# Performance work log

Hardware: AMD Instinct MI355X
Metric: run time of the kernel (lower is better)

The kernel has to match this reference:

```python
import jax, jax.numpy as jnp
import numpy as np

B, T, IN = 128, 2048, 32      # batch, seq_len, input dim
S, M = 32, 8                  # kaarma state dim, number of ensemble models
E, H = 64, 128                # encoder dim, controller GRU hidden
CIN = E + 1                   # controller input = [encoded, error]


def setup_inputs() -> dict:
    key = jax.random.key(0)
    ks = jax.random.split(key, 15)
    sc = 0.1  # small init scale keeps tanh/sigmoid in sane range
    return {
        "x": jax.random.normal(ks[0], (B, T, IN), jnp.float32),
        "y": jax.random.normal(ks[1], (B, T), jnp.float32),
        # mkaarma params: shared encoder + per-model recurrent state update
        "W_enc": jax.random.normal(ks[2], (IN, E), jnp.float32) * sc,
        "b_enc": jnp.zeros((E,), jnp.float32),
        "W_in": jax.random.normal(ks[3], (M, IN, S), jnp.float32) * sc,
        "W_rec": jax.random.normal(ks[4], (M, S, S), jnp.float32) * sc,
        "b_s": jnp.zeros((M, S), jnp.float32),
        # controller params: GRU cell + gate head
        "W_x": jax.random.normal(ks[5], (CIN, 3 * H), jnp.float32) * sc,
        "W_h": jax.random.normal(ks[6], (H, 3 * H), jnp.float32) * sc,
        "b_x": jnp.zeros((3 * H,), jnp.float32),
        "b_h": jnp.zeros((3 * H,), jnp.float32),
        "W_gate": jax.random.normal(ks[7], (H, M), jnp.float32) * sc,
        "b_gate": jnp.zeros((M,), jnp.float32),
    }


def reference(x, y, W_enc, b_enc, W_in, W_rec, b_s,
              W_x, W_h, b_x, b_h, W_gate, b_gate):
    Bv = x.shape[0]
    dt = x.dtype

    def step(carry, xy):
        kstate, h, err = carry            # [B,S], [B,H], [B]
        x_t, y_t = xy                     # [B,IN], [B]
        # mkaarma: encode input + ensemble of candidate next states
        encoded = jnp.tanh(x_t @ W_enc + b_enc)                        # [B,E]
        new_state = jnp.tanh(
            jnp.einsum('bi,mis->bms', x_t, W_in)
            + jnp.einsum('bs,msd->bmd', kstate, W_rec)
            + b_s
        )                                                              # [B,M,S]
        # controller: GRU cell on [encoded, error]
        inp = jnp.concatenate([encoded, err[:, None]], axis=1)         # [B,E+1]
        xz, xr, xn = jnp.split(inp @ W_x + b_x, 3, axis=1)
        hz, hr, hn = jnp.split(h @ W_h + b_h, 3, axis=1)
        z = jax.nn.sigmoid(xz + hz)
        r = jax.nn.sigmoid(xr + hr)
        n = jnp.tanh(xn + r * hn)
        h_new = (1.0 - z) * n + z * h                                  # [B,H]
        # gate softmax over models, mix candidate states
        gate = jax.nn.softmax(h_new @ W_gate + b_gate, axis=1)         # [B,M]
        kstate_new = jnp.einsum('bm,bms->bs', gate, new_state)         # [B,S]
        pred = kstate_new[:, -1]                                       # [B]
        err_new = pred - y_t
        return (kstate_new, h_new, err_new), pred

    init = (jnp.zeros((Bv, S), dt), jnp.zeros((Bv, H), dt), jnp.zeros((Bv,), dt))
    xs = (jnp.swapaxes(x, 0, 1), jnp.swapaxes(y, 0, 1))   # time-major
    _, preds = jax.lax.scan(step, init, xs)               # [T,B]
    return jnp.swapaxes(preds, 0, 1)                      # [B,T]
```

## Files before the change

kernel.cpp:

```cpp
#include <hip/hip_runtime.h>

typedef _Float16 h2 __attribute__((ext_vector_type(2)));
typedef _Float16 h8 __attribute__((ext_vector_type(8)));

#define NB 128
#define NT 2048
#define NIN 32
#define NS 32
#define NM 8
#define NE 64
#define NH 128
#define NH3 384

__device__ __forceinline__ h2 mkh2(float a, float b) {
  h2 r; r[0] = (_Float16)a; r[1] = (_Float16)b; return r;
}

template <int I>
__device__ __forceinline__ h2 pick2(h8 v) {
  return __builtin_shufflevector(v, v, 2 * I, 2 * I + 1);
}

__device__ __forceinline__ float fdot2(h2 a, h2 b, float c) {
#if __has_builtin(__builtin_amdgcn_fdot2)
  return __builtin_amdgcn_fdot2(a, b, c, false);
#else
  return c + (float)a[0] * (float)b[0] + (float)a[1] * (float)b[1];
#endif
}

__device__ __forceinline__ float rcpf(float v) {
#if __has_builtin(__builtin_amdgcn_rcpf)
  return __builtin_amdgcn_rcpf(v);
#else
  return 1.0f / v;
#endif
}

__device__ __forceinline__ float sigmoid_f(float v) { return rcpf(1.0f + __expf(-v)); }
__device__ __forceinline__ float tanh_f(float v) { return 1.0f - 2.0f * rcpf(1.0f + __expf(2.0f * v)); }

template <int CTRL>
__device__ __forceinline__ float dppadd(float v) {
  int t = __builtin_amdgcn_update_dpp(0, __float_as_int(v), CTRL, 0xF, 0xF, true);
  return v + __int_as_float(t);
}
__device__ __forceinline__ float wave_reduce63(float v) {
  v = dppadd<0x111>(v); v = dppadd<0x112>(v); v = dppadd<0x114>(v);
  v = dppadd<0x118>(v); v = dppadd<0x142>(v); v = dppadd<0x143>(v);
  return v;
}
__device__ __forceinline__ float pairsum(float v) {
  int t = __builtin_amdgcn_update_dpp(0, __float_as_int(v), 0xB1, 0xF, 0xF, true);
  return v + __int_as_float(t);
}

__device__ __forceinline__ void lds_fence() {
  asm volatile("s_waitcnt lgkmcnt(0)" ::: "memory");
}

#define RPW 16
__global__ __launch_bounds__(256, 1) void pre2(
    const float* __restrict__ gx, const float* __restrict__ W_enc,
    const float* __restrict__ b_enc, const float* __restrict__ W_x,
    const float* __restrict__ b_x, _Float16* __restrict__ xpre,
    _Float16* __restrict__ xh16, int t0, int CH) {
  const int tid = threadIdx.x, wv = tid >> 6, lane = tid & 63;
  __shared__ __align__(16) _Float16 x16[4][NIN];
  __shared__ __align__(16) _Float16 encA[4][RPW][NE];

  h2 we[16];
#pragma unroll
  for (int i = 0; i < 16; ++i)
    we[i] = mkh2(W_enc[(2 * i) * NE + lane], W_enc[(2 * i + 1) * NE + lane]);
  const float be = b_enc[lane];

  const int g0 = ((int)blockIdx.x * 4 + wv) * RPW;

  h2 wx3[96];
#pragma unroll 1
  for (int pass = 0; pass < 2; ++pass) {
#pragma unroll
    for (int kk = 0; kk < 3; ++kk) {
      const int j = lane + 64 * (3 * pass + kk);
#pragma unroll
      for (int i = 0; i < 32; ++i)
        wx3[kk * 32 + i] = mkh2(W_x[(size_t)(2 * i) * NH3 + j], W_x[(size_t)(2 * i + 1) * NH3 + j]);
    }
#pragma unroll 1
    for (int r = 0; r < RPW; ++r) {
      const int g = g0 + r;
      const int bb = g / CH, tc = g % CH;
      if (pass == 0) {
        const float* xr = gx + ((size_t)bb * NT + t0 + tc) * NIN;
        if (lane < NIN) x16[wv][lane] = (_Float16)xr[lane];
        lds_fence();
        if (lane < 16) {
          const unsigned v = *(const unsigned*)&x16[wv][2 * lane];
          ((unsigned*)xh16)[(size_t)g * 16 + lane] = v;
        }
        const h8* xv8 = (const h8*)x16[wv];
        float a = be;
#pragma unroll
        for (int i = 0; i < 4; ++i) {
          const h8 xv = xv8[i];
          a = fdot2(pick2<0>(xv), we[4 * i + 0], a);
          a = fdot2(pick2<1>(xv), we[4 * i + 1], a);
          a = fdot2(pick2<2>(xv), we[4 * i + 2], a);
          a = fdot2(pick2<3>(xv), we[4 * i + 3], a);
        }
        encA[wv][r][lane] = (_Float16)tanh_f(a);
        lds_fence();
      }
      const h8* ev8 = (const h8*)encA[wv][r];
      h8 ev[8];
#pragma unroll
      for (int i = 0; i < 8; ++i) ev[i] = ev8[i];
#pragma unroll
      for (int kk = 0; kk < 3; ++kk) {
        const int j = lane + 64 * (3 * pass + kk);
        float a = b_x[j], c = 0.f;
#pragma unroll
        for (int i = 0; i < 8; ++i) {
          a = fdot2(pick2<0>(ev[i]), wx3[kk * 32 + 4 * i + 0], a);
          c = fdot2(pick2<1>(ev[i]), wx3[kk * 32 + 4 * i + 1], c);
          a = fdot2(pick2<2>(ev[i]), wx3[kk * 32 + 4 * i + 2], a);
          c = fdot2(pick2<3>(ev[i]), wx3[kk * 32 + 4 * i + 3], c);
        }
        xpre[(size_t)g * NH3 + j] = (_Float16)(a + c);
      }
    }
  }
}

__global__ __launch_bounds__(384, 2) void rnn3(
    const float* __restrict__ gy, const _Float16* __restrict__ xpre,
    const _Float16* __restrict__ xh16,
    const float* __restrict__ W_h, const float* __restrict__ b_h,
    const float* __restrict__ W_in, const float* __restrict__ W_rec,
    const float* __restrict__ b_s, const float* __restrict__ W_x,
    const float* __restrict__ W_gate, const float* __restrict__ b_gate,
    float* __restrict__ out, float* __restrict__ state, int t0, int CH) {
  const int tid = threadIdx.x;
  const int b = blockIdx.x;
  const int wv = tid >> 6;
  const int lane = tid & 63;

  __shared__ __align__(16) _Float16 h_sh[2][NH];
  __shared__ __align__(16) _Float16 xpre_sh[2][NH3];
  __shared__ __align__(16) float ns_sh[2][NS][NM];
  __shared__ __align__(16) float xd_sh[2][2 * NH];
  __shared__ __align__(16) float gp_sh[2][4][NM];
  __shared__ __align__(16) _Float16 kst_sh[NS];
  __shared__ float err_sh;

  float* st = state + b * (NH + NS + 1);

  h2 wbig[96];
  h2 wrec[16];
  float wg[8];
  float bh[3], wxe[3];
  float bs4[4];
  float bg[8];
  float h_prev = 0.f;
  float yp = 0.f, ym = 0.f;
  unsigned xpa0 = 0, xpa1 = 0, xpa2 = 0, xpb0 = 0, xpb1 = 0, xpb2 = 0;
  h8 xha[4], xhb[4];

  const int gl = tid - 128;
  const int j = gl >> 1;
  const int half = gl & 1;

  if (wv >= 2) {
#pragma unroll
    for (int g = 0; g < 3; ++g) {
      const int jc = j + 128 * g;
#pragma unroll
      for (int i = 0; i < 32; ++i)
        wbig[g * 32 + i] = mkh2(W_h[(size_t)(64 * half + 2 * i) * NH3 + jc],
                                W_h[(size_t)(64 * half + 2 * i + 1) * NH3 + jc]);
      bh[g] = b_h[jc];
      wxe[g] = W_x[(size_t)NE * NH3 + jc];
    }
#pragma unroll
    for (int m = 0; m < 8; ++m) wg[m] = half ? 0.f : W_gate[j * NM + m];
    {
      const int m0 = gl >> 5, d0 = gl & 31;
#pragma unroll
      for (int i = 0; i < 16; ++i)
        wrec[i] = mkh2(W_rec[m0 * 1024 + (2 * i) * 32 + d0],
                       W_rec[m0 * 1024 + (2 * i + 1) * 32 + d0]);
    }
    h_prev = t0 ? st[j] : 0.f;
    if (!half) h_sh[1][j] = (_Float16)h_prev;
  } else if (wv == 1) {
#pragma unroll
    for (int k = 0; k < 4; ++k) {
      const int o = lane + 64 * k, m = o >> 5, d = o & 31;
#pragma unroll
      for (int i = 0; i < 16; ++i)
        wbig[k * 16 + i] = mkh2(W_in[m * 1024 + (2 * i) * 32 + d],
                                W_in[m * 1024 + (2 * i + 1) * 32 + d]);
      bs4[k] = b_s[o];
    }
    const unsigned* xpg = (const unsigned*)xpre;
    {
      const size_t r0 = (size_t)(b * CH + 0) * 192;
      xpa0 = xpg[r0 + lane]; xpa1 = xpg[r0 + lane + 64]; xpa2 = xpg[r0 + lane + 128];
      const size_t r1 = (size_t)(b * CH + min(1, CH - 1)) * 192;
      xpb0 = xpg[r1 + lane]; xpb1 = xpg[r1 + lane + 64]; xpb2 = xpg[r1 + lane + 128];
    }
    {
      const h8* x0 = (const h8*)(xh16 + (size_t)(b * CH + 0) * NIN);
      h8 xv[4];
#pragma unroll
      for (int i = 0; i < 4; ++i) xv[i] = x0[i];
#pragma unroll
      for (int k = 0; k < 4; ++k) {
        float s = bs4[k];
#pragma unroll
        for (int i = 0; i < 4; ++i) {
          s = fdot2(pick2<0>(xv[i]), wbig[k * 16 + 4 * i + 0], s);
          s = fdot2(pick2<1>(xv[i]), wbig[k * 16 + 4 * i + 1], s);
          s = fdot2(pick2<2>(xv[i]), wbig[k * 16 + 4 * i + 2], s);
          s = fdot2(pick2<3>(xv[i]), wbig[k * 16 + 4 * i + 3], s);
        }
        xd_sh[1][lane + 64 * k] = s;
      }
      const h8* x1 = (const h8*)(xh16 + (size_t)(b * CH + min(1, CH - 1)) * NIN);
      const h8* x2 = (const h8*)(xh16 + (size_t)(b * CH + min(2, CH - 1)) * NIN);
#pragma unroll
      for (int i = 0; i < 4; ++i) { xha[i] = x1[i]; xhb[i] = x2[i]; }
    }
  } else {
#pragma unroll
    for (int m = 0; m < 8; ++m) bg[m] = b_gate[m];
    if (lane < NS) kst_sh[lane] = t0 ? (_Float16)st[NH + lane] : (_Float16)0.f;
    if (lane == 0) err_sh = t0 ? st[NH + NS] : 0.f;
    yp = gy[(size_t)b * NT + t0];
    ym = gy[(size_t)b * NT + min(t0 + 1, NT - 1)];
  }
  __syncthreads();

  float hz = 0.f, hr = 0.f, hn = 0.f;

  for (int tc = 0; tc < CH; ++tc) {
    const int q = tc & 1, qp = q ^ 1;
    if (wv >= 2) {
      const h8* hv8 = (const h8*)&h_sh[qp][64 * half];
      float a0 = 0.f, c0 = 0.f, a1 = 0.f, c1 = 0.f, a2 = 0.f, c2 = 0.f;
#pragma unroll
      for (int i = 0; i < 8; ++i) {
        const h8 hv = hv8[i];
        a0 = fdot2(pick2<0>(hv), wbig[4 * i + 0], a0);
        c0 = fdot2(pick2<1>(hv), wbig[4 * i + 1], c0);
        a0 = fdot2(pick2<2>(hv), wbig[4 * i + 2], a0);
        c0 = fdot2(pick2<3>(hv), wbig[4 * i + 3], c0);
        a1 = fdot2(pick2<0>(hv), wbig[32 + 4 * i + 0], a1);
        c1 = fdot2(pick2<1>(hv), wbig[32 + 4 * i + 1], c1);
        a1 = fdot2(pick2<2>(hv), wbig[32 + 4 * i + 2], a1);
        c1 = fdot2(pick2<3>(hv), wbig[32 + 4 * i + 3], c1);
        a2 = fdot2(pick2<0>(hv), wbig[64 + 4 * i + 0], a2);
        c2 = fdot2(pick2<1>(hv), wbig[64 + 4 * i + 1], c2);
        a2 = fdot2(pick2<2>(hv), wbig[64 + 4 * i + 2], a2);
        c2 = fdot2(pick2<3>(hv), wbig[64 + 4 * i + 3], c2);
      }
      hz = pairsum(a0 + c0) + bh[0];
      hr = pairsum(a1 + c1) + bh[1];
      hn = pairsum(a2 + c2) + bh[2];
    } else if (wv == 0) {
      if (tc > 0) {
        const float4* g4 = (const float4*)&gp_sh[qp][0][0];
        float4 A = g4[0], Bv = g4[1];
        A.x += g4[2].x + g4[4].x + g4[6].x; A.y += g4[2].y + g4[4].y + g4[6].y;
        A.z += g4[2].z + g4[4].z + g4[6].z; A.w += g4[2].w + g4[4].w + g4[6].w;
        Bv.x += g4[3].x + g4[5].x + g4[7].x; Bv.y += g4[3].y + g4[5].y + g4[7].y;
        Bv.z += g4[3].z + g4[5].z + g4[7].z; Bv.w += g4[3].w + g4[5].w + g4[7].w;
        float l[8] = {A.x + bg[0], A.y + bg[1], A.z + bg[2], A.w + bg[3],
                      Bv.x + bg[4], Bv.y + bg[5], Bv.z + bg[6], Bv.w + bg[7]};
        float mx = fmaxf(fmaxf(fmaxf(l[0], l[1]), fmaxf(l[2], l[3])),
                         fmaxf(fmaxf(l[4], l[5]), fmaxf(l[6], l[7])));
        float e[8], s = 0.f;
#pragma unroll
        for (int m = 0; m < 8; ++m) { e[m] = __expf(l[m] - mx); s += e[m]; }
        const int u = lane & 31;
        const float4* nsv = (const float4*)&ns_sh[qp][u][0];
        const float4 n0 = nsv[0], n1 = nsv[1];
        float ks = e[0] * n0.x + e[1] * n0.y + e[2] * n0.z + e[3] * n0.w +
                   e[4] * n1.x + e[5] * n1.y + e[6] * n1.z + e[7] * n1.w;
        ks *= rcpf(s);
        if (lane < NS) kst_sh[u] = (_Float16)ks;
        if (lane == 31) {
          out[(size_t)b * NT + t0 + tc - 1] = ks;
          err_sh = ks - yp;
        }
        yp = ym;
        ym = gy[(size_t)b * NT + min(t0 + tc + 1, NT - 1)];
      }
    } else {
      unsigned* xps = (unsigned*)&xpre_sh[q][0];
      xps[lane] = xpa0; xps[lane + 64] = xpa1; xps[lane + 128] = xpa2;
      xpa0 = xpb0; xpa1 = xpb1; xpa2 = xpb2;
      const unsigned* xpg = (const unsigned*)xpre;
      const size_t rn = (size_t)(b * CH + min(tc + 2, CH - 1)) * 192;
      xpb0 = xpg[rn + lane]; xpb1 = xpg[rn + lane + 64]; xpb2 = xpg[rn + lane + 128];
    }
    __syncthreads();
    if (wv >= 2) {
      const float err = err_sh;
      const float xz = (float)xpre_sh[q][j] + err * wxe[0];
      const float xr = (float)xpre_sh[q][j + 128] + err * wxe[1];
      const float xn = (float)xpre_sh[q][j + 256] + err * wxe[2];
      const float z = sigmoid_f(hz + xz);
      const float r = sigmoid_f(hr + xr);
      const float n = tanh_f(xn + r * hn);
      const float hnew = (1.f - z) * n + z * h_prev;
      h_prev = hnew;
      if (!half) h_sh[q][j] = (_Float16)hnew;
      float p[8];
#pragma unroll
      for (int m = 0; m < 8; ++m) p[m] = wave_reduce63(hnew * wg[m]);
      if (lane == 63) {
        *(float4*)&gp_sh[q][wv - 2][0] = make_float4(p[0], p[1], p[2], p[3]);
        *(float4*)&gp_sh[q][wv - 2][4] = make_float4(p[4], p[5], p[6], p[7]);
      }
      const h8* kv8 = (const h8*)kst_sh;
      float s = xd_sh[qp][gl];
#pragma unroll
      for (int i = 0; i < 4; ++i) {
        const h8 kv = kv8[i];
        s = fdot2(pick2<0>(kv), wrec[4 * i + 0], s);
        s = fdot2(pick2<1>(kv), wrec[4 * i + 1], s);
        s = fdot2(pick2<2>(kv), wrec[4 * i + 2], s);
        s = fdot2(pick2<3>(kv), wrec[4 * i + 3], s);
      }
      ns_sh[q][gl & 31][gl >> 5] = tanh_f(s);
    } else if (wv == 1) {
      if (tc + 1 < CH) {
#pragma unroll
        for (int k = 0; k < 4; ++k) {
          float s = bs4[k];
#pragma unroll
          for (int i = 0; i < 4; ++i) {
            s = fdot2(pick2<0>(xha[i]), wbig[k * 16 + 4 * i + 0], s);
            s = fdot2(pick2<1>(xha[i]), wbig[k * 16 + 4 * i + 1], s);
            s = fdot2(pick2<2>(xha[i]), wbig[k * 16 + 4 * i + 2], s);
            s = fdot2(pick2<3>(xha[i]), wbig[k * 16 + 4 * i + 3], s);
          }
          xd_sh[q][lane + 64 * k] = s;
        }
      }
#pragma unroll
      for (int i = 0; i < 4; ++i) xha[i] = xhb[i];
      const h8* xn8 = (const h8*)(xh16 + (size_t)(b * CH + min(tc + 3, CH - 1)) * NIN);
#pragma unroll
      for (int i = 0; i < 4; ++i) xhb[i] = xn8[i];
    }
    __syncthreads();
  }

  if (wv == 0) {
    const int qf = (CH - 1) & 1;
    const float4* g4 = (const float4*)&gp_sh[qf][0][0];
    float4 A = g4[0], Bv = g4[1];
    A.x += g4[2].x + g4[4].x + g4[6].x; A.y += g4[2].y + g4[4].y + g4[6].y;
    A.z += g4[2].z + g4[4].z + g4[6].z; A.w += g4[2].w + g4[4].w + g4[6].w;
    Bv.x += g4[3].x + g4[5].x + g4[7].x; Bv.y += g4[3].y + g4[5].y + g4[7].y;
    Bv.z += g4[3].z + g4[5].z + g4[7].z; Bv.w += g4[3].w + g4[5].w + g4[7].w;
    float l[8] = {A.x + bg[0], A.y + bg[1], A.z + bg[2], A.w + bg[3],
                  Bv.x + bg[4], Bv.y + bg[5], Bv.z + bg[6], Bv.w + bg[7]};
    float mx = fmaxf(fmaxf(fmaxf(l[0], l[1]), fmaxf(l[2], l[3])),
                     fmaxf(fmaxf(l[4], l[5]), fmaxf(l[6], l[7])));
    float e[8], s = 0.f;
#pragma unroll
    for (int m = 0; m < 8; ++m) { e[m] = __expf(l[m] - mx); s += e[m]; }
    const int u = lane & 31;
    const float4* nsv = (const float4*)&ns_sh[qf][u][0];
    const float4 n0 = nsv[0], n1 = nsv[1];
    float ks = e[0] * n0.x + e[1] * n0.y + e[2] * n0.z + e[3] * n0.w +
               e[4] * n1.x + e[5] * n1.y + e[6] * n1.z + e[7] * n1.w;
    ks *= rcpf(s);
    if (lane < NS) st[NH + u] = ks;
    if (lane == 31) {
      out[(size_t)b * NT + t0 + CH - 1] = ks;
      st[NH + NS] = ks - yp;
    }
  }
  if (wv >= 2 && !half) st[j] = h_prev;
}

extern "C" void kernel_launch(void* const* d_in, const int* in_sizes, int n_in,
                              void* d_out, int out_size, void* d_ws, size_t ws_size,
                              hipStream_t stream) {
  const float* x = (const float*)d_in[0];
  const float* y = (const float*)d_in[1];
  const float* W_enc = (const float*)d_in[2];
  const float* b_enc = (const float*)d_in[3];
  const float* W_in = (const float*)d_in[4];
  const float* W_rec = (const float*)d_in[5];
  const float* b_s = (const float*)d_in[6];
  const float* W_x = (const float*)d_in[7];
  const float* W_h = (const float*)d_in[8];
  const float* b_x = (const float*)d_in[9];
  const float* b_h = (const float*)d_in[10];
  const float* W_gate = (const float*)d_in[11];
  const float* b_gate = (const float*)d_in[12];
  float* out = (float*)d_out;

  const size_t stateB = (size_t)NB * (NH + NS + 1) * sizeof(float);
  int CH = NT;
  while (CH > 1) {
    const size_t need = (size_t)NB * CH * NH3 * 2 + (size_t)NB * CH * NIN * 2 + stateB;
    if (need <= ws_size) break;
    CH >>= 1;
  }

  _Float16* xpre = (_Float16*)d_ws;
  _Float16* xh16 = (_Float16*)((char*)d_ws + (size_t)NB * CH * NH3 * 2);
  float* state = (float*)((char*)d_ws + (size_t)NB * CH * NH3 * 2 + (size_t)NB * CH * NIN * 2);

  for (int t0 = 0; t0 < NT; t0 += CH) {
    pre2<<<dim3(2 * CH), dim3(256), 0, stream>>>(
        x, W_enc, b_enc, W_x, b_x, xpre, xh16, t0, CH);
    rnn3<<<dim3(NB), dim3(384), 0, stream>>>(
        y, xpre, xh16, W_h, b_h, W_in, W_rec, b_s, W_x, W_gate, b_gate,
        out, state, t0, CH);
  }
}
```

Measured before the change: 2.715 ms.

## Unroll recurrence by four steps with batched prefetch and LDS-staged targets

The per-step loop is unrolled four times via a macro, so the loader wave fetches four timesteps of precomputed GRU inputs and encoded x rows in one batch instead of a rolling two-deep register prefetch. The target sequence y for the chunk is staged into shared memory up front, which removes the per-step global load of y on the critical wave. This trades more registers and 8KB of extra LDS for fewer dependent global loads per step. The minimum chunk size becomes 4 because the loop assumes CH is a multiple of 4.

```diff
diff --git a/kernel.cpp b/kernel.cpp
--- a/kernel.cpp
+++ b/kernel.cpp
@@ -133,7 +133,7 @@
   }
 }
 
-__global__ __launch_bounds__(384, 2) void rnn3(
+__global__ __launch_bounds__(384, 2) void rnn7(
     const float* __restrict__ gy, const _Float16* __restrict__ xpre,
     const _Float16* __restrict__ xh16,
     const float* __restrict__ W_h, const float* __restrict__ b_h,
@@ -153,6 +153,7 @@
   __shared__ __align__(16) float gp_sh[2][4][NM];
   __shared__ __align__(16) _Float16 kst_sh[NS];
   __shared__ float err_sh;
+  __shared__ float y_lds[NT];
 
   float* st = state + b * (NH + NS + 1);
 
@@ -163,13 +164,14 @@
   float bs4[4];
   float bg[8];
   float h_prev = 0.f;
-  float yp = 0.f, ym = 0.f;
-  unsigned xpa0 = 0, xpa1 = 0, xpa2 = 0, xpb0 = 0, xpb1 = 0, xpb2 = 0;
-  h8 xha[4], xhb[4];
+  unsigned xpq[12];
+  h8 xr0[4], xr1[4], xr2[4], xr3[4];
 
   const int gl = tid - 128;
   const int j = gl >> 1;
   const int half = gl & 1;
+
+  for (int i = tid; i < CH; i += 384) y_lds[i] = gy[(size_t)b * NT + t0 + i];
 
   if (wv >= 2) {
 #pragma unroll
@@ -203,164 +205,174 @@
                                 W_in[m * 1024 + (2 * i + 1) * 32 + d]);
       bs4[k] = b_s[o];
     }
-    const unsigned* xpg = (const unsigned*)xpre;
     {
-      const size_t r0 = (size_t)(b * CH + 0) * 192;
-      xpa0 = xpg[r0 + lane]; xpa1 = xpg[r0 + lane + 64]; xpa2 = xpg[r0 + lane + 128];
-      const size_t r1 = (size_t)(b * CH + min(1, CH - 1)) * 192;
-      xpb0 = xpg[r1 + lane]; xpb1 = xpg[r1 + lane + 64]; xpb2 = xpg[r1 + lane + 128];
-    }
-    {
-      const h8* x0 = (const h8*)(xh16 + (size_t)(b * CH + 0) * NIN);
-      h8 xv[4];
-#pragma unroll
-      for (int i = 0; i < 4; ++i) xv[i] = x0[i];
+      const h8* x0 = (const h8*)(xh16 + (size_t)(b * CH) * NIN);
+#pragma unroll
+      for (int i = 0; i < 4; ++i) xr0[i] = x0[i];
 #pragma unroll
       for (int k = 0; k < 4; ++k) {
         float s = bs4[k];
 #pragma unroll
         for (int i = 0; i < 4; ++i) {
-          s = fdot2(pick2<0>(xv[i]), wbig[k * 16 + 4 * i + 0], s);
-          s = fdot2(pick2<1>(xv[i]), wbig[k * 16 + 4 * i + 1], s);
-          s = fdot2(pick2<2>(xv[i]), wbig[k * 16 + 4 * i + 2], s);
-          s = fdot2(pick2<3>(xv[i]), wbig[k * 16 + 4 * i + 3], s);
+          s = fdot2(pick2<0>(xr0[i]), wbig[k * 16 + 4 * i + 0], s);
+          s = fdot2(pick2<1>(xr0[i]), wbig[k * 16 + 4 * i + 1], s);
+          s = fdot2(pick2<2>(xr0[i]), wbig[k * 16 + 4 * i + 2], s);
+          s = fdot2(pick2<3>(xr0[i]), wbig[k * 16 + 4 * i + 3], s);
         }
         xd_sh[1][lane + 64 * k] = s;
       }
-      const h8* x1 = (const h8*)(xh16 + (size_t)(b * CH + min(1, CH - 1)) * NIN);
-      const h8* x2 = (const h8*)(xh16 + (size_t)(b * CH + min(2, CH - 1)) * NIN);
-#pragma unroll
-      for (int i = 0; i < 4; ++i) { xha[i] = x1[i]; xhb[i] = x2[i]; }
     }
   } else {
 #pragma unroll
     for (int m = 0; m < 8; ++m) bg[m] = b_gate[m];
     if (lane < NS) kst_sh[lane] = t0 ? (_Float16)st[NH + lane] : (_Float16)0.f;
     if (lane == 0) err_sh = t0 ? st[NH + NS] : 0.f;
-    yp = gy[(size_t)b * NT + t0];
-    ym = gy[(size_t)b * NT + min(t0 + 1, NT - 1)];
   }
   __syncthreads();
 
   float hz = 0.f, hr = 0.f, hn = 0.f;
 
-  for (int tc = 0; tc < CH; ++tc) {
-    const int q = tc & 1, qp = q ^ 1;
-    if (wv >= 2) {
-      const h8* hv8 = (const h8*)&h_sh[qp][64 * half];
-      float a0 = 0.f, c0 = 0.f, a1 = 0.f, c1 = 0.f, a2 = 0.f, c2 = 0.f;
-#pragma unroll
-      for (int i = 0; i < 8; ++i) {
-        const h8 hv = hv8[i];
-        a0 = fdot2(pick2<0>(hv), wbig[4 * i + 0], a0);
-        c0 = fdot2(pick2<1>(hv), wbig[4 * i + 1], c0);
-        a0 = fdot2(pick2<2>(hv), wbig[4 * i + 2], a0);
-        c0 = fdot2(pick2<3>(hv), wbig[4 * i + 3], c0);
-        a1 = fdot2(pick2<0>(hv), wbig[32 + 4 * i + 0], a1);
-        c1 = fdot2(pick2<1>(hv), wbig[32 + 4 * i + 1], c1);
-        a1 = fdot2(pick2<2>(hv), wbig[32 + 4 * i + 2], a1);
-        c1 = fdot2(pick2<3>(hv), wbig[32 + 4 * i + 3], c1);
-        a2 = fdot2(pick2<0>(hv), wbig[64 + 4 * i + 0], a2);
-        c2 = fdot2(pick2<1>(hv), wbig[64 + 4 * i + 1], c2);
-        a2 = fdot2(pick2<2>(hv), wbig[64 + 4 * i + 2], a2);
-        c2 = fdot2(pick2<3>(hv), wbig[64 + 4 * i + 3], c2);
-      }
-      hz = pairsum(a0 + c0) + bh[0];
-      hr = pairsum(a1 + c1) + bh[1];
-      hn = pairsum(a2 + c2) + bh[2];
-    } else if (wv == 0) {
-      if (tc > 0) {
-        const float4* g4 = (const float4*)&gp_sh[qp][0][0];
-        float4 A = g4[0], Bv = g4[1];
-        A.x += g4[2].x + g4[4].x + g4[6].x; A.y += g4[2].y + g4[4].y + g4[6].y;
-        A.z += g4[2].z + g4[4].z + g4[6].z; A.w += g4[2].w + g4[4].w + g4[6].w;
-        Bv.x += g4[3].x + g4[5].x + g4[7].x; Bv.y += g4[3].y + g4[5].y + g4[7].y;
-        Bv.z += g4[3].z + g4[5].z + g4[7].z; Bv.w += g4[3].w + g4[5].w + g4[7].w;
-        float l[8] = {A.x + bg[0], A.y + bg[1], A.z + bg[2], A.w + bg[3],
-                      Bv.x + bg[4], Bv.y + bg[5], Bv.z + bg[6], Bv.w + bg[7]};
-        float mx = fmaxf(fmaxf(fmaxf(l[0], l[1]), fmaxf(l[2], l[3])),
-                         fmaxf(fmaxf(l[4], l[5]), fmaxf(l[6], l[7])));
-        float e[8], s = 0.f;
-#pragma unroll
-        for (int m = 0; m < 8; ++m) { e[m] = __expf(l[m] - mx); s += e[m]; }
-        const int u = lane & 31;
-        const float4* nsv = (const float4*)&ns_sh[qp][u][0];
-        const float4 n0 = nsv[0], n1 = nsv[1];
-        float ks = e[0] * n0.x + e[1] * n0.y + e[2] * n0.z + e[3] * n0.w +
-                   e[4] * n1.x + e[5] * n1.y + e[6] * n1.z + e[7] * n1.w;
-        ks *= rcpf(s);
-        if (lane < NS) kst_sh[u] = (_Float16)ks;
-        if (lane == 31) {
-          out[(size_t)b * NT + t0 + tc - 1] = ks;
-          err_sh = ks - yp;
-        }
-        yp = ym;
-        ym = gy[(size_t)b * NT + min(t0 + tc + 1, NT - 1)];
-      }
-    } else {
-      unsigned* xps = (unsigned*)&xpre_sh[q][0];
-      xps[lane] = xpa0; xps[lane + 64] = xpa1; xps[lane + 128] = xpa2;
-      xpa0 = xpb0; xpa1 = xpb1; xpa2 = xpb2;
-      const unsigned* xpg = (const unsigned*)xpre;
-      const size_t rn = (size_t)(b * CH + min(tc + 2, CH - 1)) * 192;
-      xpb0 = xpg[rn + lane]; xpb1 = xpg[rn + lane + 64]; xpb2 = xpg[rn + lane + 128];
-    }
-    __syncthreads();
-    if (wv >= 2) {
-      const float err = err_sh;
-      const float xz = (float)xpre_sh[q][j] + err * wxe[0];
-      const float xr = (float)xpre_sh[q][j + 128] + err * wxe[1];
-      const float xn = (float)xpre_sh[q][j + 256] + err * wxe[2];
-      const float z = sigmoid_f(hz + xz);
-      const float r = sigmoid_f(hr + xr);
-      const float n = tanh_f(xn + r * hn);
-      const float hnew = (1.f - z) * n + z * h_prev;
-      h_prev = hnew;
-      if (!half) h_sh[q][j] = (_Float16)hnew;
-      float p[8];
-#pragma unroll
-      for (int m = 0; m < 8; ++m) p[m] = wave_reduce63(hnew * wg[m]);
-      if (lane == 63) {
-        *(float4*)&gp_sh[q][wv - 2][0] = make_float4(p[0], p[1], p[2], p[3]);
-        *(float4*)&gp_sh[q][wv - 2][4] = make_float4(p[4], p[5], p[6], p[7]);
-      }
-      const h8* kv8 = (const h8*)kst_sh;
-      float s = xd_sh[qp][gl];
-#pragma unroll
-      for (int i = 0; i < 4; ++i) {
-        const h8 kv = kv8[i];
-        s = fdot2(pick2<0>(kv), wrec[4 * i + 0], s);
-        s = fdot2(pick2<1>(kv), wrec[4 * i + 1], s);
-        s = fdot2(pick2<2>(kv), wrec[4 * i + 2], s);
-        s = fdot2(pick2<3>(kv), wrec[4 * i + 3], s);
-      }
-      ns_sh[q][gl & 31][gl >> 5] = tanh_f(s);
-    } else if (wv == 1) {
-      if (tc + 1 < CH) {
-#pragma unroll
-        for (int k = 0; k < 4; ++k) {
-          float s = bs4[k];
-#pragma unroll
-          for (int i = 0; i < 4; ++i) {
-            s = fdot2(pick2<0>(xha[i]), wbig[k * 16 + 4 * i + 0], s);
-            s = fdot2(pick2<1>(xha[i]), wbig[k * 16 + 4 * i + 1], s);
-            s = fdot2(pick2<2>(xha[i]), wbig[k * 16 + 4 * i + 2], s);
-            s = fdot2(pick2<3>(xha[i]), wbig[k * 16 + 4 * i + 3], s);
-          }
-          xd_sh[q][lane + 64 * k] = s;
-        }
-      }
-#pragma unroll
-      for (int i = 0; i < 4; ++i) xha[i] = xhb[i];
-      const h8* xn8 = (const h8*)(xh16 + (size_t)(b * CH + min(tc + 3, CH - 1)) * NIN);
-#pragma unroll
-      for (int i = 0; i < 4; ++i) xhb[i] = xn8[i];
-    }
-    __syncthreads();
-  }
+#define STEPK(K, XRK)                                                          \
+  {                                                                            \
+    const int tc = tc4 + (K);                                                  \
+    const int q = (K) & 1, qp = q ^ 1;                                         \
+                                 \
+    if (wv >= 2) {                                                             \
+      const h8* hv8 = (const h8*)&h_sh[qp][64 * half];                         \
+      float a0 = 0.f, c0 = 0.f, a1 = 0.f, c1 = 0.f, a2 = 0.f, c2 = 0.f;        \
+      _Pragma("unroll")                                                        \
+      for (int i = 0; i < 8; ++i) {                                            \
+        const h8 hv = hv8[i];                                                  \
+        a0 = fdot2(pick2<0>(hv), wbig[4 * i + 0], a0);                         \
+        c0 = fdot2(pick2<1>(hv), wbig[4 * i + 1], c0);                         \
+        a0 = fdot2(pick2<2>(hv), wbig[4 * i + 2], a0);                         \
+        c0 = fdot2(pick2<3>(hv), wbig[4 * i + 3], c0);                         \
+        a1 = fdot2(pick2<0>(hv), wbig[32 + 4 * i + 0], a1);                    \
+        c1 = fdot2(pick2<1>(hv), wbig[32 + 4 * i + 1], c1);                    \
+        a1 = fdot2(pick2<2>(hv), wbig[32 + 4 * i + 2], a1);                    \
+        c1 = fdot2(pick2<3>(hv), wbig[32 + 4 * i + 3], c1);                    \
+        a2 = fdot2(pick2<0>(hv), wbig[64 + 4 * i + 0], a2);                    \
+        c2 = fdot2(pick2<1>(hv), wbig[64 + 4 * i + 1], c2);                    \
+        a2 = fdot2(pick2<2>(hv), wbig[64 + 4 * i + 2], a2);                    \
+        c2 = fdot2(pick2<3>(hv), wbig[64 + 4 * i + 3], c2);                    \
+      }                                                                        \
+      hz = pairsum(a0 + c0) + bh[0];                                           \
+      hr = pairsum(a1 + c1) + bh[1];                                           \
+      hn = pairsum(a2 + c2) + bh[2];                                           \
+    } else if (wv == 0) {                                                      \
+      if (tc > 0) {                                                            \
+        const int u = lane & 31;                                               \
+        const float4* nsv = (const float4*)&ns_sh[qp][u][0];                   \
+        const float4 n0 = nsv[0], n1 = nsv[1];                                 \
+        const float4* g4 = (const float4*)&gp_sh[qp][0][0];                    \
+        float4 A = g4[0], Bv = g4[1];                                          \
+        A.x += g4[2].x + g4[4].x + g4[6].x; A.y += g4[2].y + g4[4].y + g4[6].y;\
+        A.z += g4[2].z + g4[4].z + g4[6].z; A.w += g4[2].w + g4[4].w + g4[6].w;\
+        Bv.x += g4[3].x + g4[5].x + g4[7].x; Bv.y += g4[3].y + g4[5].y + g4[7].y;\
+        Bv.z += g4[3].z + g4[5].z + g4[7].z; Bv.w += g4[3].w + g4[5].w + g4[7].w;\
+        float l[8] = {A.x + bg[0], A.y + bg[1], A.z + bg[2], A.w + bg[3],      \
+                      Bv.x + bg[4], Bv.y + bg[5], Bv.z + bg[6], Bv.w + bg[7]}; \
+        float mx = fmaxf(fmaxf(fmaxf(l[0], l[1]), fmaxf(l[2], l[3])),          \
+                         fmaxf(fmaxf(l[4], l[5]), fmaxf(l[6], l[7])));         \
+        float e[8], s = 0.f;                                                   \
+        _Pragma("unroll")                                                      \
+        for (int m = 0; m < 8; ++m) { e[m] = __expf(l[m] - mx); s += e[m]; }   \
+        float ks = e[0] * n0.x + e[1] * n0.y + e[2] * n0.z + e[3] * n0.w +     \
+                   e[4] * n1.x + e[5] * n1.y + e[6] * n1.z + e[7] * n1.w;      \
+        ks *= rcpf(s);                                                         \
+        if (lane < NS) kst_sh[u] = (_Float16)ks;                               \
+        if (lane == 31) {                                                      \
+          out[(size_t)b * NT + t0 + tc - 1] = ks;                              \
+          err_sh = ks - y_lds[tc - 1];                                         \
+        }                                                                      \
+      }                                                                        \
+    } else {    \
+      if ((K) == 0) {                                                          \
+        const unsigned* xpg = (const unsigned*)xpre;                           \
+        _Pragma("unroll")                                                      \
+        for (int k = 0; k < 4; ++k) {                                          \
+          const size_t rr = (size_t)(b * CH + tc4 + k) * 192;                  \
+          xpq[3 * k + 0] = xpg[rr + lane];                                     \
+          xpq[3 * k + 1] = xpg[rr + lane + 64];                                \
+          xpq[3 * k + 2] = xpg[rr + lane + 128];                               \
+        }                                                                      \
+        const h8* xg0 = (const h8*)(xh16 + (size_t)(b * CH + min(tc4 + 1, CH - 1)) * NIN); \
+        const h8* xg1 = (const h8*)(xh16 + (size_t)(b * CH + min(tc4 + 2, CH - 1)) * NIN); \
+        const h8* xg2 = (const h8*)(xh16 + (size_t)(b * CH + min(tc4 + 3, CH - 1)) * NIN); \
+        const h8* xg3 = (const h8*)(xh16 + (size_t)(b * CH + min(tc4 + 4, CH - 1)) * NIN); \
+        _Pragma("unroll")                                                      \
+        for (int i = 0; i < 4; ++i) {                                          \
+          xr0[i] = xg0[i]; xr1[i] = xg1[i]; xr2[i] = xg2[i]; xr3[i] = xg3[i];  \
+        }                                                                      \
+      }                                                                        \
+      unsigned* xps = (unsigned*)&xpre_sh[q][0];                               \
+      xps[lane] = xpq[3 * (K) + 0];                                            \
+      xps[lane + 64] = xpq[3 * (K) + 1];                                       \
+      xps[lane + 128] = xpq[3 * (K) + 2];                                      \
+    }                                                                          \
+    __syncthreads();                                                           \
+                                 \
+    if (wv >= 2) {                                                             \
+      const float err = err_sh;                                                \
+      const float xz = (float)xpre_sh[q][j] + err * wxe[0];                    \
+      const float xr = (float)xpre_sh[q][j + 128] + err * wxe[1];              \
+      const float xn = (float)xpre_sh[q][j + 256] + err * wxe[2];              \
+      const float z = sigmoid_f(hz + xz);                                      \
+      const float r = sigmoid_f(hr + xr);                                      \
+      const float n = tanh_f(xn + r * hn);                                     \
+      const float hnew = (1.f - z) * n + z * h_prev;                           \
+      h_prev = hnew;                                                           \
+      if (!half) h_sh[q][j] = (_Float16)hnew;                                  \
+      float p[8];                                                              \
+      _Pragma("unroll")                                                        \
+      for (int m = 0; m < 8; ++m) p[m] = wave_reduce63(hnew * wg[m]);          \
+      if (lane == 63) {                                                        \
+        *(float4*)&gp_sh[q][wv - 2][0] = make_float4(p[0], p[1], p[2], p[3]);  \
+        *(float4*)&gp_sh[q][wv - 2][4] = make_float4(p[4], p[5], p[6], p[7]);  \
+      }                                                                        \
+      const h8* kv8 = (const h8*)kst_sh;                                       \
+      float s = xd_sh[qp][gl];                                                 \
+      _Pragma("unroll")                                                        \
+      for (int i = 0; i < 4; ++i) {                                            \
+        const h8 kv = kv8[i];                                                  \
+        s = fdot2(pick2<0>(kv), wrec[4 * i + 0], s);                           \
+        s = fdot2(pick2<1>(kv), wrec[4 * i + 1], s);                           \
+        s = fdot2(pick2<2>(kv), wrec[4 * i + 2], s);                           \
+        s = fdot2(pick2<3>(kv), wrec[4 * i + 3], s);                           \
+      }                                                                        \
+      ns_sh[q][gl & 31][gl >> 5] = tanh_f(s);                                  \
+    } else if (wv == 1) {                                                      \
+      if (tc + 1 < CH) {                                                       \
+        _Pragma("unroll")                                                      \
+        for (int k = 0; k < 4; ++k) {                                          \
+          float s = bs4[k];                                                    \
+          _Pragma("unroll")                                                    \
+          for (int i = 0; i < 4; ++i) {                                        \
+            s = fdot2(pick2<0>(XRK[i]), wbig[k * 16 + 4 * i + 0], s);          \
+            s = fdot2(pick2<1>(XRK[i]), wbig[k * 16 + 4 * i + 1], s);          \
+            s = fdot2(pick2<2>(XRK[i]), wbig[k * 16 + 4 * i + 2], s);          \
+            s = fdot2(pick2<3>(XRK[i]), wbig[k * 16 + 4 * i + 3], s);          \
+          }                                                                    \
+          xd_sh[q][lane + 64 * k] = s;                                         \
+        }                                                                      \
+      }                                                                        \
+    }                                                                          \
+    __syncthreads();                                                           \
+  }
+
+  for (int tc4 = 0; tc4 < CH; tc4 += 4) {
+    STEPK(0, xr0)
+    STEPK(1, xr1)
+    STEPK(2, xr2)
+    STEPK(3, xr3)
+  }
+#undef STEPK
 
   if (wv == 0) {
     const int qf = (CH - 1) & 1;
+    const int u = lane & 31;
+    const float4* nsv = (const float4*)&ns_sh[qf][u][0];
+    const float4 n0 = nsv[0], n1 = nsv[1];
     const float4* g4 = (const float4*)&gp_sh[qf][0][0];
     float4 A = g4[0], Bv = g4[1];
     A.x += g4[2].x + g4[4].x + g4[6].x; A.y += g4[2].y + g4[4].y + g4[6].y;
@@ -374,16 +386,13 @@
     float e[8], s = 0.f;
 #pragma unroll
     for (int m = 0; m < 8; ++m) { e[m] = __expf(l[m] - mx); s += e[m]; }
-    const int u = lane & 31;
-    const float4* nsv = (const float4*)&ns_sh[qf][u][0];
-    const float4 n0 = nsv[0], n1 = nsv[1];
     float ks = e[0] * n0.x + e[1] * n0.y + e[2] * n0.z + e[3] * n0.w +
                e[4] * n1.x + e[5] * n1.y + e[6] * n1.z + e[7] * n1.w;
     ks *= rcpf(s);
     if (lane < NS) st[NH + u] = ks;
     if (lane == 31) {
       out[(size_t)b * NT + t0 + CH - 1] = ks;
-      st[NH + NS] = ks - yp;
+      st[NH + NS] = ks - y_lds[CH - 1];
     }
   }
   if (wv >= 2 && !half) st[j] = h_prev;
@@ -409,7 +418,7 @@
 
   const size_t stateB = (size_t)NB * (NH + NS + 1) * sizeof(float);
   int CH = NT;
-  while (CH > 1) {
+  while (CH > 4) {
     const size_t need = (size_t)NB * CH * NH3 * 2 + (size_t)NB * CH * NIN * 2 + stateB;
     if (need <= ws_size) break;
     CH >>= 1;
@@ -422,7 +431,7 @@
   for (int t0 = 0; t0 < NT; t0 += CH) {
     pre2<<<dim3(2 * CH), dim3(256), 0, stream>>>(
         x, W_enc, b_enc, W_x, b_x, xpre, xh16, t0, CH);
-    rnn3<<<dim3(NB), dim3(384), 0, stream>>>(
+    rnn7<<<dim3(NB), dim3(384), 0, stream>>>(
         y, xpre, xh16, W_h, b_h, W_in, W_rec, b_s, W_x, W_gate, b_gate,
         out, state, t0, CH);
   }
```

Measured after the change: 2.591 ms. 4.6% less time.
